# Optimization experiments

Measured on AMD Instinct MI355X. Metric: run time of the kernel, lower is better.

The kernel has to match this reference:

```python
import jax, jax.numpy as jnp
import numpy as np

N, DIM = 512, 64
SIZE, QUANT = 3.0, 0.25
LXY = int((2 * SIZE + 1e-4) // QUANT)   # 24
LZ = int((2 * 2 + 1e-4) // QUANT)       # 16


def setup_inputs() -> dict:
    key = jax.random.key(0)
    ks = jax.random.split(key, 16)
    s = lambda d: 1.0 / np.sqrt(d)
    feat = jax.random.normal(ks[0], (N, DIM), jnp.float32)
    dxy = jax.random.uniform(ks[1], (N, N, 2), jnp.float32, -SIZE, SIZE)
    dz = jax.random.uniform(ks[2], (N, N, 1), jnp.float32, -2.0, 2.0)
    distance = jnp.concatenate([dxy, dz], axis=-1)
    return {
        "feat": feat,
        "distance": distance,
        "W_qkv": jax.random.normal(ks[3], (DIM, 3 * DIM), jnp.float32) * s(DIM),
        "b_qkv": jnp.zeros((3 * DIM,), jnp.float32),
        "Wg1": jax.random.normal(ks[4], (DIM, DIM), jnp.float32) * s(DIM),
        "bg1": jnp.zeros((DIM,), jnp.float32),
        "Wg2": jax.random.normal(ks[5], (DIM, DIM), jnp.float32) * s(DIM),
        "bg2": jnp.zeros((DIM,), jnp.float32),
        "table_x": jax.random.normal(ks[6], (3, LXY, DIM), jnp.float32) * 0.02,
        "table_y": jax.random.normal(ks[7], (3, LXY, DIM), jnp.float32) * 0.02,
        "table_z": jax.random.normal(ks[8], (3, LZ, DIM), jnp.float32) * 0.02,
        "Wd": jax.random.normal(ks[9], (3 * DIM, DIM), jnp.float32) * s(3 * DIM),
        "bd": jnp.zeros((DIM,), jnp.float32),
        "ln_g": jnp.ones((DIM,), jnp.float32),
        "ln_b": jnp.zeros((DIM,), jnp.float32),
    }


def _quant_idx(distance):
    ixy = jnp.minimum((distance[:, :, :2] + SIZE) // QUANT, 2.0 * SIZE / QUANT - 1)
    iz = jnp.minimum((distance[:, :, 2:] + 2.0) // QUANT, 4.0 / QUANT - 1)
    return jnp.concatenate([ixy, iz], axis=-1).astype(jnp.int32)  # [N,N,3]


def _vec_att(feat, idx, W_qkv, b_qkv, Wg1, bg1, Wg2, bg2, table_x, table_y, table_z):
    n, dim = feat.shape
    qkv = (feat @ W_qkv + b_qkv).reshape(n, 3, dim)
    q, k, v = qkv[:, 0], qkv[:, 1], qkv[:, 2]
    # relation MLP on pairwise q-k differences: [N,N,dim]
    rel = q[:, None, :] - k[None, :, :]
    rel = jnp.maximum(rel @ Wg1 + bg1, 0.0) @ Wg2 + bg2
    ix, iy, iz = idx[:, :, 0], idx[:, :, 1], idx[:, :, 2]
    enc_q = table_x[0][ix] + table_y[0][iy] + table_z[0][iz]
    enc_k = table_x[1][ix] + table_y[1][iy] + table_z[1][iz]
    enc_v = table_x[2][ix] + table_y[2][iy] + table_z[2][iz]
    rel = rel + q[:, None, :] * enc_q + k[None, :, :] * enc_k
    vv = v[None, :, :] + enc_v
    weights = jax.nn.softmax(rel, axis=1)
    return jnp.sum(weights * vv, axis=1)  # [N,dim]


def reference(feat, distance, W_qkv, b_qkv, Wg1, bg1, Wg2, bg2,
              table_x, table_y, table_z, Wd, bd, ln_g, ln_b):
    idx = _quant_idx(distance)
    att = _vec_att(feat, idx, W_qkv, b_qkv, Wg1, bg1, Wg2, bg2,
                   table_x, table_y, table_z)
    n = att.shape[0]
    mean_rep = jnp.broadcast_to(jnp.mean(att, axis=0, keepdims=True), att.shape)
    max_rep = jnp.broadcast_to(jnp.max(att, axis=0, keepdims=True), att.shape)
    x = jnp.concatenate([att, mean_rep, max_rep], axis=-1)  # [N, 3*dim]
    h = x @ Wd + bd
    mu = jnp.mean(h, axis=-1, keepdims=True)
    var = jnp.mean((h - mu) ** 2, axis=-1, keepdims=True)
    h = (h - mu) * jax.lax.rsqrt(var + 1e-5) * ln_g + ln_b
    return jnp.maximum(h, 0.0)
```

## Files before the change

### kernel.cpp

```cpp
#include <hip/hip_runtime.h>
#include <hip/hip_bf16.h>
#include <math.h>

#define N 512
#define DIM 64

typedef __attribute__((ext_vector_type(8))) short short8;
typedef __attribute__((ext_vector_type(4))) float f32x4;

#define WS_Q 0
#define WS_B (N*DIM)
#define WS_A (2*N*DIM)
#define WS_ATT (3*N*DIM)
#define WS_MEAN (4*N*DIM)
#define WS_MAXK (4*N*DIM + DIM)
#define WS_KV (4*N*DIM + 2*DIM)

__device__ __forceinline__ unsigned short f2bf(float f) {
    unsigned u = __float_as_uint(f);
    return (unsigned short)((u + 0x7fffu + ((u >> 16) & 1u)) >> 16);
}

__device__ __forceinline__ float fexp2(float x) {
    float r;
    asm("v_exp_f32 %0, %1" : "=v"(r) : "v"(x));
    return r;
}

__global__ void k_qkv(const float* __restrict__ feat, const float* __restrict__ Wqkv,
                      const float* __restrict__ bqkv, const float* __restrict__ Wg1,
                      const float* __restrict__ bg1, float* __restrict__ ws) {
    __shared__ float frow[DIM];
    __shared__ float qrow[DIM];
    __shared__ float krow[DIM];
    __shared__ float vrow[DIM];
    int i = blockIdx.x;
    int c = threadIdx.x;
    if (i == 0 && c < DIM) {
        ws[WS_MEAN + c] = 0.0f;
        ((unsigned*)ws)[WS_MAXK + c] = 0u;
    }
    if (c < DIM) frow[c] = feat[i * DIM + c];
    __syncthreads();
    float a0 = bqkv[c], a1 = 0.f, a2 = 0.f, a3 = 0.f;
#pragma unroll
    for (int kk = 0; kk < DIM; kk += 4) {
        a0 += frow[kk + 0] * Wqkv[(kk + 0) * 3 * DIM + c];
        a1 += frow[kk + 1] * Wqkv[(kk + 1) * 3 * DIM + c];
        a2 += frow[kk + 2] * Wqkv[(kk + 2) * 3 * DIM + c];
        a3 += frow[kk + 3] * Wqkv[(kk + 3) * 3 * DIM + c];
    }
    float acc = (a0 + a1) + (a2 + a3);
    if (c < DIM) {
        ws[WS_Q + i * DIM + c] = acc;
        qrow[c] = acc;
    } else if (c < 2 * DIM) {
        krow[c - DIM] = acc;
    } else {
        vrow[c - 2 * DIM] = acc;
    }
    __syncthreads();
    if (c < DIM) {
        float b0 = bg1[c], b1 = 0.f, b2 = 0.f, b3 = 0.f;
#pragma unroll
    for (int kk = 0; kk < DIM; kk += 4) {
            b0 += qrow[kk + 0] * Wg1[(kk + 0) * DIM + c];
            b1 += qrow[kk + 1] * Wg1[(kk + 1) * DIM + c];
            b2 += qrow[kk + 2] * Wg1[(kk + 2) * DIM + c];
            b3 += qrow[kk + 3] * Wg1[(kk + 3) * DIM + c];
        }
        ws[WS_A + i * DIM + c] = (b0 + b1) + (b2 + b3);
    } else if (c < 2 * DIM) {
        int cc = c - DIM;
        float b0 = 0.f, b1 = 0.f, b2 = 0.f, b3 = 0.f;
#pragma unroll
        for (int kk = 0; kk < DIM; kk += 4) {
            b0 += krow[kk + 0] * Wg1[(kk + 0) * DIM + cc];
            b1 += krow[kk + 1] * Wg1[(kk + 1) * DIM + cc];
            b2 += krow[kk + 2] * Wg1[(kk + 2) * DIM + cc];
            b3 += krow[kk + 3] * Wg1[(kk + 3) * DIM + cc];
        }
        ws[WS_B + i * DIM + cc] = (b0 + b1) + (b2 + b3);
    } else {
        int cc = c - 2 * DIM;
        ((unsigned*)ws)[WS_KV + i * DIM + cc] =
            ((unsigned)f2bf(krow[cc]) << 16) | (unsigned)f2bf(vrow[cc]);
    }
}

__global__ __launch_bounds__(512, 2) void k_attn(
    const float* __restrict__ dist,
    const float* __restrict__ tx, const float* __restrict__ ty,
    const float* __restrict__ tz, const float* __restrict__ Wg2,
    const float* __restrict__ bg2, float* __restrict__ ws) {
    __shared__ uint2 sxp[24 * 65];
    __shared__ uint2 syp[24 * 65];
    __shared__ uint2 szp[16 * 65];
    __shared__ int sidx[N];
    __shared__ float smrg[8][4][16][2];

    const int i = blockIdx.x;
    const int tid = threadIdx.x;
    const int w = tid >> 6;
    const int lane = tid & 63;
    const int l15 = lane & 15;
    const int kg = lane >> 4;
    const float LOG2E = 1.4426950408889634f;

    for (int t = tid; t < 24 * 64; t += 512) {
        int row = t >> 6, d = t & 63, o = row * 65 + d;
        sxp[o] = make_uint2((__float_as_uint(tx[t]) & 0xffff0000u) |
                            (__float_as_uint(tx[1536 + t] * LOG2E) >> 16),
                            __float_as_uint(tx[3072 + t]));
        syp[o] = make_uint2((__float_as_uint(ty[t]) & 0xffff0000u) |
                            (__float_as_uint(ty[1536 + t] * LOG2E) >> 16),
                            __float_as_uint(ty[3072 + t]));
    }
    for (int t = tid; t < 16 * 64; t += 512) {
        int row = t >> 6, d = t & 63, o = row * 65 + d;
        szp[o] = make_uint2((__float_as_uint(tz[t]) & 0xffff0000u) |
                            (__float_as_uint(tz[1024 + t] * LOG2E) >> 16),
                            __float_as_uint(tz[2048 + t]));
    }
    for (int j = tid; j < N; j += 512) {
        const float* dp = dist + ((size_t)i * N + j) * 3;
        int ix = min((int)floorf((dp[0] + 3.0f) * 4.0f), 23);
        int iy = min((int)floorf((dp[1] + 3.0f) * 4.0f), 23);
        int iz = min((int)floorf((dp[2] + 2.0f) * 4.0f), 15);
        sidx[j] = ix | (iy << 5) | (iz << 10);
    }

    short8 wB[4][2];
#pragma unroll
    for (int n = 0; n < 4; ++n)
#pragma unroll
        for (int ks = 0; ks < 2; ++ks) {
            union { short8 v; unsigned short u[8]; } tmp;
#pragma unroll
            for (int e = 0; e < 8; ++e)
                tmp.u[e] = f2bf(Wg2[(ks * 32 + kg * 8 + e) * DIM + n * 16 + l15] * LOG2E);
            wB[n][ks] = tmp.v;
        }
    float af[2][8];
    {
        const float* ap = ws + WS_A + i * DIM + kg * 8;
#pragma unroll
        for (int ks = 0; ks < 2; ++ks)
#pragma unroll
            for (int e = 0; e < 8; ++e) af[ks][e] = ap[ks * 32 + e];
    }
    float qr[4], br[4];
#pragma unroll
    for (int n = 0; n < 4; ++n) {
        qr[n] = ws[WS_Q + i * DIM + n * 16 + l15] * LOG2E;
        br[n] = bg2[n * 16 + l15] * LOG2E;
    }

    const float* Bp = ws + WS_B;
    const unsigned* kvp = (const unsigned*)ws + WS_KV;

    float stl[4] = {0.f, 0.f, 0.f, 0.f};
    float sta[4] = {0.f, 0.f, 0.f, 0.f};
    __syncthreads();

#pragma unroll 2
    for (int t4 = 0; t4 < 4; ++t4) {
        const int j0w = (w + 8 * t4) * 16;
        short8 h[2];
        {
            const float* bb = Bp + (j0w + l15) * DIM + kg * 8;
#pragma unroll
            for (int ks = 0; ks < 2; ++ks) {
                union { short8 v; unsigned short u[8]; } hh;
#pragma unroll
                for (int e = 0; e < 8; ++e)
                    hh.u[e] = f2bf(fmaxf(af[ks][e] - bb[ks * 32 + e], 0.f));
                h[ks] = hh.v;
            }
        }
        f32x4 acc[4];
#pragma unroll
        for (int n = 0; n < 4; ++n) {
            acc[n] = (f32x4)(br[n]);
            acc[n] = __builtin_amdgcn_mfma_f32_16x16x32_bf16(h[0], wB[n][0], acc[n], 0, 0, 0);
            acc[n] = __builtin_amdgcn_mfma_f32_16x16x32_bf16(h[1], wB[n][1], acc[n], 0, 0, 0);
        }
        int pk[4];
#pragma unroll
        for (int rr = 0; rr < 4; ++rr) pk[rr] = sidx[j0w + kg * 4 + rr];
#pragma unroll
        for (int n = 0; n < 4; ++n) {
            const int dof = n * 16 + l15;
#pragma unroll
            for (int rr = 0; rr < 4; ++rr) {
                int ix = pk[rr] & 31, iy = (pk[rr] >> 5) & 31, iz = pk[rr] >> 10;
                uint2 gx = sxp[ix * 65 + dof];
                uint2 gy = syp[iy * 65 + dof];
                uint2 gz = szp[iz * 65 + dof];
                float eq = __uint_as_float(gx.x & 0xffff0000u) +
                           __uint_as_float(gy.x & 0xffff0000u) +
                           __uint_as_float(gz.x & 0xffff0000u);
                float ek = __uint_as_float(gx.x << 16) +
                           __uint_as_float(gy.x << 16) +
                           __uint_as_float(gz.x << 16);
                float ev = __uint_as_float(gx.y) + __uint_as_float(gy.y) +
                           __uint_as_float(gz.y);
                int j = j0w + kg * 4 + rr;
                unsigned ukv = kvp[j * DIM + dof];
                float kv = __uint_as_float(ukv & 0xffff0000u);
                float vv = __uint_as_float(ukv << 16);
                float rel2 = acc[n][rr] + qr[n] * eq + kv * ek;
                float p = fexp2(rel2);
                stl[n] += p;
                sta[n] = fmaf(p, vv + ev, sta[n]);
            }
        }
    }

#pragma unroll
    for (int n = 0; n < 4; ++n) {
#pragma unroll
        for (int off = 16; off <= 32; off <<= 1) {
            stl[n] += __shfl_xor(stl[n], off);
            sta[n] += __shfl_xor(sta[n], off);
        }
        if (lane < 16) {
            smrg[w][n][l15][0] = stl[n];
            smrg[w][n][l15][1] = sta[n];
        }
    }
    __syncthreads();
    if (tid < DIM) {
        int n = tid >> 4, c = tid & 15;
        float l = 0.f, a = 0.f;
#pragma unroll
        for (int ww = 0; ww < 8; ++ww) {
            l += smrg[ww][n][c][0];
            a += smrg[ww][n][c][1];
        }
        float att = a / l;
        ws[WS_ATT + i * DIM + tid] = att;
        atomicAdd(ws + WS_MEAN + tid, att);
        unsigned u = __float_as_uint(att);
        unsigned key = (u & 0x80000000u) ? ~u : (u | 0x80000000u);
        atomicMax((unsigned*)ws + WS_MAXK + tid, key);
    }
}

__global__ void k_final(const float* __restrict__ ws, const float* __restrict__ Wd,
                        const float* __restrict__ bd, const float* __restrict__ lng,
                        const float* __restrict__ lnb, float* __restrict__ out) {
    __shared__ float xs[3 * DIM];
    __shared__ float hp[4][DIM];
    int i = blockIdx.x;
    int tid = threadIdx.x;
    int c = tid & 63, q = tid >> 6;
    if (tid < DIM) xs[tid] = ws[WS_ATT + i * DIM + tid];
    else if (tid < 2 * DIM) xs[tid] = ws[WS_MEAN + (tid - DIM)] * (1.0f / (float)N);
    else if (tid < 3 * DIM) {
        unsigned key = ((const unsigned*)ws)[WS_MAXK + (tid - 2 * DIM)];
        unsigned ub = (key & 0x80000000u) ? (key & 0x7fffffffu) : ~key;
        xs[tid] = __uint_as_float(ub);
    }
    __syncthreads();
    float p0 = (q == 0) ? bd[c] : 0.0f, p1 = 0.f;
#pragma unroll
    for (int kk = q * 48; kk < q * 48 + 48; kk += 2) {
        p0 += xs[kk] * Wd[kk * DIM + c];
        p1 += xs[kk + 1] * Wd[(kk + 1) * DIM + c];
    }
    hp[q][c] = p0 + p1;
    __syncthreads();
    if (tid < DIM) {
        float h = hp[0][tid] + hp[1][tid] + hp[2][tid] + hp[3][tid];
        float s = h;
#pragma unroll
        for (int off = 32; off >= 1; off >>= 1) s += __shfl_xor(s, off);
        float mu = s * (1.0f / DIM);
        float dif = h - mu;
        float s2 = dif * dif;
#pragma unroll
        for (int off = 32; off >= 1; off >>= 1) s2 += __shfl_xor(s2, off);
        float var = s2 * (1.0f / DIM);
        float rs = rsqrtf(var + 1e-5f);
        float o = dif * rs * lng[tid] + lnb[tid];
        out[i * DIM + tid] = fmaxf(o, 0.0f);
    }
}

extern "C" void kernel_launch(void* const* d_in, const int* in_sizes, int n_in,
                              void* d_out, int out_size, void* d_ws, size_t ws_size,
                              hipStream_t stream) {
    (void)in_sizes; (void)n_in; (void)out_size; (void)ws_size;
    const float* feat = (const float*)d_in[0];
    const float* dist = (const float*)d_in[1];
    const float* Wqkv = (const float*)d_in[2];
    const float* bqkv = (const float*)d_in[3];
    const float* Wg1  = (const float*)d_in[4];
    const float* bg1  = (const float*)d_in[5];
    const float* Wg2  = (const float*)d_in[6];
    const float* bg2  = (const float*)d_in[7];
    const float* tx   = (const float*)d_in[8];
    const float* ty   = (const float*)d_in[9];
    const float* tz   = (const float*)d_in[10];
    const float* Wd   = (const float*)d_in[11];
    const float* bd   = (const float*)d_in[12];
    const float* lng  = (const float*)d_in[13];
    const float* lnb  = (const float*)d_in[14];
    float* ws = (float*)d_ws;
    float* out = (float*)d_out;

    hipLaunchKernelGGL(k_qkv, dim3(N), dim3(192), 0, stream, feat, Wqkv, bqkv, Wg1, bg1, ws);
    hipLaunchKernelGGL(k_attn, dim3(N), dim3(512), 0, stream, dist, tx, ty, tz, Wg2, bg2, ws);
    hipLaunchKernelGGL(k_final, dim3(N), dim3(256), 0, stream, ws, Wd, bd, lng, lnb, out);
}
```

Before: 130.9 us.

## Replace LDS table gathers with one-hot MFMA products for positional encodings

The three per-element shared-memory gathers of the x/y/z encoding tables are replaced by matrix-core multiplications. A bf16 one-hot matrix built from the quantized indices multiplies register-resident concatenated tables, with q pre-folded into the Q table and LOG2E into the K table. Table staging now copies raw fp32 tables into a single 64-row shared array, and the launch-bounds minimum-blocks hint is dropped. This trades LDS gather traffic and scalar adds for six extra MFMAs per tile and many more live registers (fQ/fK/fV fragments), which may lower occupancy. The encodings are also rounded to bf16, losing precision.

```diff
diff --git a/kernel.cpp b/kernel.cpp
--- a/kernel.cpp
+++ b/kernel.cpp
@@ -63,7 +63,7 @@
     if (c < DIM) {
         float b0 = bg1[c], b1 = 0.f, b2 = 0.f, b3 = 0.f;
 #pragma unroll
-    for (int kk = 0; kk < DIM; kk += 4) {
+        for (int kk = 0; kk < DIM; kk += 4) {
             b0 += qrow[kk + 0] * Wg1[(kk + 0) * DIM + c];
             b1 += qrow[kk + 1] * Wg1[(kk + 1) * DIM + c];
             b2 += qrow[kk + 2] * Wg1[(kk + 2) * DIM + c];
@@ -88,14 +88,12 @@
     }
 }
 
-__global__ __launch_bounds__(512, 2) void k_attn(
+__global__ __launch_bounds__(512) void k_attn(
     const float* __restrict__ dist,
     const float* __restrict__ tx, const float* __restrict__ ty,
     const float* __restrict__ tz, const float* __restrict__ Wg2,
     const float* __restrict__ bg2, float* __restrict__ ws) {
-    __shared__ uint2 sxp[24 * 65];
-    __shared__ uint2 syp[24 * 65];
-    __shared__ uint2 szp[16 * 65];
+    __shared__ float sT[3 * 64 * 64];
     __shared__ int sidx[N];
     __shared__ float smrg[8][4][16][2];
 
@@ -107,40 +105,22 @@
     const int kg = lane >> 4;
     const float LOG2E = 1.4426950408889634f;
 
-    for (int t = tid; t < 24 * 64; t += 512) {
-        int row = t >> 6, d = t & 63, o = row * 65 + d;
-        sxp[o] = make_uint2((__float_as_uint(tx[t]) & 0xffff0000u) |
-                            (__float_as_uint(tx[1536 + t] * LOG2E) >> 16),
-                            __float_as_uint(tx[3072 + t]));
-        syp[o] = make_uint2((__float_as_uint(ty[t]) & 0xffff0000u) |
-                            (__float_as_uint(ty[1536 + t] * LOG2E) >> 16),
-                            __float_as_uint(ty[3072 + t]));
-    }
-    for (int t = tid; t < 16 * 64; t += 512) {
-        int row = t >> 6, d = t & 63, o = row * 65 + d;
-        szp[o] = make_uint2((__float_as_uint(tz[t]) & 0xffff0000u) |
-                            (__float_as_uint(tz[1024 + t] * LOG2E) >> 16),
-                            __float_as_uint(tz[2048 + t]));
+    for (int t = tid; t < 3 * 64 * 64; t += 512) {
+        int set = t >> 12, r = (t >> 6) & 63, d = t & 63;
+        float v;
+        if (r < 24)      v = tx[set * 1536 + r * 64 + d];
+        else if (r < 48) v = ty[set * 1536 + (r - 24) * 64 + d];
+        else             v = tz[set * 1024 + (r - 48) * 64 + d];
+        sT[t] = v;
     }
     for (int j = tid; j < N; j += 512) {
         const float* dp = dist + ((size_t)i * N + j) * 3;
         int ix = min((int)floorf((dp[0] + 3.0f) * 4.0f), 23);
         int iy = min((int)floorf((dp[1] + 3.0f) * 4.0f), 23);
         int iz = min((int)floorf((dp[2] + 2.0f) * 4.0f), 15);
-        sidx[j] = ix | (iy << 5) | (iz << 10);
-    }
-
-    short8 wB[4][2];
-#pragma unroll
-    for (int n = 0; n < 4; ++n)
-#pragma unroll
-        for (int ks = 0; ks < 2; ++ks) {
-            union { short8 v; unsigned short u[8]; } tmp;
-#pragma unroll
-            for (int e = 0; e < 8; ++e)
-                tmp.u[e] = f2bf(Wg2[(ks * 32 + kg * 8 + e) * DIM + n * 16 + l15] * LOG2E);
-            wB[n][ks] = tmp.v;
-        }
+        sidx[j] = ix | ((24 + iy) << 6) | ((48 + iz) << 12);
+    }
+
     float af[2][8];
     {
         const float* ap = ws + WS_A + i * DIM + kg * 8;
@@ -149,11 +129,35 @@
 #pragma unroll
             for (int e = 0; e < 8; ++e) af[ks][e] = ap[ks * 32 + e];
     }
-    float qr[4], br[4];
+    float qrn[4], brn[4];
 #pragma unroll
     for (int n = 0; n < 4; ++n) {
-        qr[n] = ws[WS_Q + i * DIM + n * 16 + l15] * LOG2E;
-        br[n] = bg2[n * 16 + l15] * LOG2E;
+        qrn[n] = ws[WS_Q + i * DIM + n * 16 + l15] * LOG2E;
+        brn[n] = bg2[n * 16 + l15] * LOG2E;
+    }
+
+    __syncthreads();
+
+    short8 wB[4][2], fQ[4][2], fK[4][2], fV[4][2];
+#pragma unroll
+    for (int n = 0; n < 4; ++n) {
+        const int dof = n * 16 + l15;
+#pragma unroll
+        for (int ks = 0; ks < 2; ++ks) {
+            union { short8 v; unsigned short u[8]; } tw, tq, tk, tv;
+#pragma unroll
+            for (int e = 0; e < 8; ++e) {
+                int k = ks * 32 + kg * 8 + e;
+                tw.u[e] = f2bf(Wg2[k * DIM + dof] * LOG2E);
+                float t0 = sT[0 * 4096 + k * 64 + dof];
+                float t1 = sT[1 * 4096 + k * 64 + dof];
+                float t2 = sT[2 * 4096 + k * 64 + dof];
+                tq.u[e] = f2bf(t0 * qrn[n]);
+                tk.u[e] = f2bf(t1 * LOG2E);
+                tv.u[e] = f2bf(t2);
+            }
+            wB[n][ks] = tw.v; fQ[n][ks] = tq.v; fK[n][ks] = tk.v; fV[n][ks] = tv.v;
+        }
     }
 
     const float* Bp = ws + WS_B;
@@ -161,7 +165,6 @@
 
     float stl[4] = {0.f, 0.f, 0.f, 0.f};
     float sta[4] = {0.f, 0.f, 0.f, 0.f};
-    __syncthreads();
 
 #pragma unroll 2
     for (int t4 = 0; t4 < 4; ++t4) {
@@ -178,41 +181,47 @@
                 h[ks] = hh.v;
             }
         }
-        f32x4 acc[4];
-#pragma unroll
-        for (int n = 0; n < 4; ++n) {
-            acc[n] = (f32x4)(br[n]);
-            acc[n] = __builtin_amdgcn_mfma_f32_16x16x32_bf16(h[0], wB[n][0], acc[n], 0, 0, 0);
-            acc[n] = __builtin_amdgcn_mfma_f32_16x16x32_bf16(h[1], wB[n][1], acc[n], 0, 0, 0);
-        }
-        int pk[4];
-#pragma unroll
-        for (int rr = 0; rr < 4; ++rr) pk[rr] = sidx[j0w + kg * 4 + rr];
+        short8 Aoh[2];
+        {
+            int pk = sidx[j0w + l15];
+            int sx = pk & 63, sy = (pk >> 6) & 63, sz = pk >> 12;
+#pragma unroll
+            for (int ks = 0; ks < 2; ++ks) {
+                union { short8 v; unsigned short u[8]; } aa;
+#pragma unroll
+                for (int e = 0; e < 8; ++e) {
+                    int k = ks * 32 + kg * 8 + e;
+                    int sel = (k < 24) ? sx : (k < 48) ? sy : sz;
+                    aa.u[e] = (sel == k) ? (unsigned short)0x3F80 : (unsigned short)0;
+                }
+                Aoh[ks] = aa.v;
+            }
+        }
 #pragma unroll
         for (int n = 0; n < 4; ++n) {
             const int dof = n * 16 + l15;
+            f32x4 aW = (f32x4)(brn[n]);
+            aW = __builtin_amdgcn_mfma_f32_16x16x32_bf16(h[0], wB[n][0], aW, 0, 0, 0);
+            aW = __builtin_amdgcn_mfma_f32_16x16x32_bf16(h[1], wB[n][1], aW, 0, 0, 0);
+            f32x4 aQ = (f32x4)(0.f);
+            aQ = __builtin_amdgcn_mfma_f32_16x16x32_bf16(Aoh[0], fQ[n][0], aQ, 0, 0, 0);
+            aQ = __builtin_amdgcn_mfma_f32_16x16x32_bf16(Aoh[1], fQ[n][1], aQ, 0, 0, 0);
+            f32x4 aK = (f32x4)(0.f);
+            aK = __builtin_amdgcn_mfma_f32_16x16x32_bf16(Aoh[0], fK[n][0], aK, 0, 0, 0);
+            aK = __builtin_amdgcn_mfma_f32_16x16x32_bf16(Aoh[1], fK[n][1], aK, 0, 0, 0);
+            f32x4 aV = (f32x4)(0.f);
+            aV = __builtin_amdgcn_mfma_f32_16x16x32_bf16(Aoh[0], fV[n][0], aV, 0, 0, 0);
+            aV = __builtin_amdgcn_mfma_f32_16x16x32_bf16(Aoh[1], fV[n][1], aV, 0, 0, 0);
 #pragma unroll
             for (int rr = 0; rr < 4; ++rr) {
-                int ix = pk[rr] & 31, iy = (pk[rr] >> 5) & 31, iz = pk[rr] >> 10;
-                uint2 gx = sxp[ix * 65 + dof];
-                uint2 gy = syp[iy * 65 + dof];
-                uint2 gz = szp[iz * 65 + dof];
-                float eq = __uint_as_float(gx.x & 0xffff0000u) +
-                           __uint_as_float(gy.x & 0xffff0000u) +
-                           __uint_as_float(gz.x & 0xffff0000u);
-                float ek = __uint_as_float(gx.x << 16) +
-                           __uint_as_float(gy.x << 16) +
-                           __uint_as_float(gz.x << 16);
-                float ev = __uint_as_float(gx.y) + __uint_as_float(gy.y) +
-                           __uint_as_float(gz.y);
                 int j = j0w + kg * 4 + rr;
                 unsigned ukv = kvp[j * DIM + dof];
                 float kv = __uint_as_float(ukv & 0xffff0000u);
                 float vv = __uint_as_float(ukv << 16);
-                float rel2 = acc[n][rr] + qr[n] * eq + kv * ek;
+                float rel2 = aW[rr] + aQ[rr] + kv * aK[rr];
                 float p = fexp2(rel2);
                 stl[n] += p;
-                sta[n] = fmaf(p, vv + ev, sta[n]);
+                sta[n] = fmaf(p, vv + aV[rr], sta[n]);
             }
         }
     }
```

Measured after the change: 236.9 us. 1.81x slower.
